# Kernel tuning notes

Measured on AMD Instinct MI355X. Metric: run time of the kernel, lower is better.

## Reference

```python
import jax, jax.numpy as jnp
import numpy as np

N_NODES = 100000
N_EDGES = 1600000
N_CLIQUES = 250000
HIDDEN = 128
HEADS = 4
D_K = 32          # attention_ratio
ATT_DIM = HEADS * D_K  # 128


def setup_inputs() -> dict:
    key = jax.random.key(0)
    ks = jax.random.split(key, 12)
    x = jax.random.normal(ks[0], (N_NODES, HIDDEN), dtype=jnp.float32)
    edge_index = jax.random.randint(ks[1], (2, N_EDGES), 0, N_NODES)
    d0_index = jax.random.randint(ks[2], (2, 2 * N_EDGES), 0, N_NODES)
    twoClique_index = jax.random.randint(ks[3], (3, N_CLIQUES), 0, N_NODES)
    d1_index = jax.random.randint(ks[4], (2, 3 * N_CLIQUES), 0, N_EDGES)
    # learned params (torch nn.Linear uses W [out,in]; we store transposed [in,out])
    scale = 0.01
    Qw = jax.random.normal(ks[5], (HIDDEN, ATT_DIM), dtype=jnp.float32) * scale
    Qb = jax.random.normal(ks[6], (ATT_DIM,), dtype=jnp.float32) * scale
    Kw = jax.random.normal(ks[7], (HIDDEN, ATT_DIM), dtype=jnp.float32) * scale
    Kb = jax.random.normal(ks[8], (ATT_DIM,), dtype=jnp.float32) * scale
    Vw = jax.random.normal(ks[9], (HIDDEN, ATT_DIM), dtype=jnp.float32) * scale
    Vb = jax.random.normal(ks[10], (ATT_DIM,), dtype=jnp.float32) * scale
    return {"x": x, "edge_index": edge_index, "d0_index": d0_index,
            "twoClique_index": twoClique_index, "d1_index": d1_index,
            "Qw": Qw, "Qb": Qb, "Kw": Kw, "Kb": Kb, "Vw": Vw, "Vb": Vb}


def reference(x, edge_index, d0_index, twoClique_index, d1_index,
              Qw, Qb, Kw, Kb, Vw, Vb):
    # projections: [N, H, d_k]
    q = (x @ Qw + Qb).reshape(-1, HEADS, D_K)
    k = (x @ Kw + Kb).reshape(-1, HEADS, D_K)
    v = (x @ Vw + Vb).reshape(-1, HEADS, D_K)

    i, j, kk = twoClique_index[0], twoClique_index[1], twoClique_index[2]
    q_i, q_j, q_k = q[i], q[j], q[kk]
    k_i, k_j, k_k = k[i], k[j], k[kk]
    v_i, v_j, v_k = v[i], v[j], v[kk]

    # symmetrized 6-term contraction, sum over d_k then mean over heads
    pre = (q_i * k_j * v_k + q_j * k_k * v_i + q_k * k_i * v_j
           + q_j * k_i * v_k + q_k * k_j * v_i + q_i * k_k * v_j).sum(-1) * (1.0 / 6.0)
    pre = pre.mean(axis=-1)            # [nCliques]
    diagA2 = jnp.exp(pre)              # use_squareplus=False

    # clique -> edge: each clique contributes its score to its 3 edges
    clique_score_per_edge = jnp.repeat(diagA2, 3)           # [3*nCliques]
    diagA1 = jax.ops.segment_sum(clique_score_per_edge, d1_index[1],
                                 num_segments=edge_index.shape[1])

    # edge -> node: each edge contributes its score to its 2 endpoints
    edge_score_per_node = jnp.repeat(diagA1, 2)             # [2*nEdges]
    diagA0 = jax.ops.segment_sum(edge_score_per_node, d0_index[1],
                                 num_segments=N_NODES)
    return (diagA0, diagA1, diagA2)
```

## Files before the change

### kernel.cpp

```cpp
#include <hip/hip_runtime.h>

#define N_NODES   100000
#define N_EDGES   1600000
#define N_CLIQUES 250000
#define FIXSCALE  8388608.0f
#define INVSCALE  1.1920928955078125e-7f

typedef unsigned short ushort8v __attribute__((ext_vector_type(8)));
typedef __bf16 bf16x8 __attribute__((ext_vector_type(8)));
typedef float f32x4 __attribute__((ext_vector_type(4)));
typedef float f32x2 __attribute__((ext_vector_type(2)));

__device__ __forceinline__ float bf2f(unsigned short u) {
    return __uint_as_float(((unsigned int)u) << 16);
}
__device__ __forceinline__ unsigned short f2bf(float f) {
    unsigned int u = __float_as_uint(f);
    u += 0x7FFFu + ((u >> 16) & 1u);
    return (unsigned short)(u >> 16);
}

__global__ __launch_bounds__(256) void prep_weights(
    const float* __restrict__ Qw, const float* __restrict__ Kw,
    const float* __restrict__ Vw, unsigned short* __restrict__ wt)
{
    int idx = blockIdx.x * 256 + threadIdx.x;
    int t = idx >> 14;
    int rem = idx & 16383;
    int col = rem >> 7;
    int k = rem & 127;
    const float* W = (t == 0) ? Qw : ((t == 1) ? Kw : Vw);
    wt[idx] = f2bf(W[k * 128 + col]);
}

__global__ __launch_bounds__(256) void proj_mfma(
    const float* __restrict__ x,
    const unsigned short* __restrict__ wt,
    const float* __restrict__ Qb, const float* __restrict__ Kb,
    const float* __restrict__ Vb,
    unsigned char* __restrict__ qkv8)
{
    __shared__ unsigned short wS[128 * 128];

    const int tid  = threadIdx.x;
    const int lane = tid & 63;
    const int w    = tid >> 6;
    const int node0 = blockIdx.x * 64;
    const int arow = lane & 15;
    const int kg   = lane >> 4;

    bf16x8 afrag[4];
    const int myNode = node0 + w * 16 + arow;
    const bool valid = myNode < N_NODES;
    const float* xrow = x + (size_t)myNode * 128;
    #pragma unroll
    for (int kt = 0; kt < 4; ++kt) {
        float4 v0, v1;
        const int kbase = kt * 32 + kg * 8;
        if (valid) {
            v0 = *(const float4*)(xrow + kbase);
            v1 = *(const float4*)(xrow + kbase + 4);
        } else {
            v0.x = v0.y = v0.z = v0.w = 0.f;
            v1.x = v1.y = v1.z = v1.w = 0.f;
        }
        ushort8v u;
        u[0] = f2bf(v0.x); u[1] = f2bf(v0.y); u[2] = f2bf(v0.z); u[3] = f2bf(v0.w);
        u[4] = f2bf(v1.x); u[5] = f2bf(v1.y); u[6] = f2bf(v1.z); u[7] = f2bf(v1.w);
        afrag[kt] = __builtin_bit_cast(bf16x8, u);
    }

    float biasr[3][8];
    #pragma unroll
    for (int t = 0; t < 3; ++t) {
        const float* Bp = (t == 0) ? Qb : ((t == 1) ? Kb : Vb);
        #pragma unroll
        for (int c = 0; c < 8; ++c) biasr[t][c] = Bp[c * 16 + arow];
    }

    for (int t = 0; t < 3; ++t) {
        __syncthreads();
        {
            const unsigned short* src = wt + t * 16384;
            #pragma unroll
            for (int it = 0; it < 8; ++it) {
                int i   = tid + it * 256;
                int col = i >> 4;
                int ko  = i & 15;
                *(ushort8v*)&wS[col * 128 + (ko ^ (col & 7)) * 8] =
                    *(const ushort8v*)(src + i * 8);
            }
        }
        __syncthreads();

        f32x4 acc[8];
        #pragma unroll
        for (int c = 0; c < 8; ++c) acc[c] = (f32x4){0.f, 0.f, 0.f, 0.f};

        #pragma unroll
        for (int kt = 0; kt < 4; ++kt) {
            const int chunk = kt * 4 + kg;
            #pragma unroll
            for (int c = 0; c < 8; ++c) {
                const int col = c * 16 + arow;
                ushort8v bu = *(const ushort8v*)&wS[col * 128 + (chunk ^ (col & 7)) * 8];
                acc[c] = __builtin_amdgcn_mfma_f32_16x16x32_bf16(
                    afrag[kt], __builtin_bit_cast(bf16x8, bu), acc[c], 0, 0, 0);
            }
        }

        #pragma unroll
        for (int r = 0; r < 4; ++r) {
            int node = node0 + w * 16 + kg * 4 + r;
            if (node < N_NODES) {
                int lo0 = __builtin_amdgcn_cvt_pk_fp8_f32(
                    acc[0][r] + biasr[t][0], acc[1][r] + biasr[t][1], 0, false);
                unsigned int w0 = (unsigned int)__builtin_amdgcn_cvt_pk_fp8_f32(
                    acc[2][r] + biasr[t][2], acc[3][r] + biasr[t][3], lo0, true);
                int lo1 = __builtin_amdgcn_cvt_pk_fp8_f32(
                    acc[4][r] + biasr[t][4], acc[5][r] + biasr[t][5], 0, false);
                unsigned int w1 = (unsigned int)__builtin_amdgcn_cvt_pk_fp8_f32(
                    acc[6][r] + biasr[t][6], acc[7][r] + biasr[t][7], lo1, true);
                uint2 o; o.x = w0; o.y = w1;
                *(uint2*)(qkv8 + (size_t)node * 384 + t * 128 + arow * 8) = o;
            }
        }
    }
}

#define DEC4(w_, a_) { f32x2 lo_ = __builtin_amdgcn_cvt_pk_f32_fp8((int)(w_), false); \
                       f32x2 hi_ = __builtin_amdgcn_cvt_pk_f32_fp8((int)(w_), true);  \
                       a_[0] = lo_[0]; a_[1] = lo_[1]; a_[2] = hi_[0]; a_[3] = hi_[1]; }

__global__ __launch_bounds__(256) void clique_kernel(
    const unsigned char* __restrict__ qkv8,
    const int* __restrict__ tci,
    const int* __restrict__ d1row1,
    const int* __restrict__ d0row1,
    float* __restrict__ outA1,
    float* __restrict__ outA2,
    unsigned int* __restrict__ a0c)
{
    const int tid = threadIdx.x;
    const int lane8 = tid & 7;
    const int cliq = (blockIdx.x * 256 + tid) >> 3;
    if (cliq >= N_CLIQUES) return;

    const int ni = tci[cliq];
    const int nj = tci[N_CLIQUES + cliq];
    const int nk = tci[2 * N_CLIQUES + cliq];
    const int d0 = lane8 * 16;

    const unsigned char* bi = qkv8 + (size_t)ni * 384 + d0;
    const unsigned char* bj = qkv8 + (size_t)nj * 384 + d0;
    const unsigned char* bk = qkv8 + (size_t)nk * 384 + d0;

    const uint4 rQi = *(const uint4*)(bi);
    const uint4 rKi = *(const uint4*)(bi + 128);
    const uint4 rVi = *(const uint4*)(bi + 256);
    const uint4 rQj = *(const uint4*)(bj);
    const uint4 rKj = *(const uint4*)(bj + 128);
    const uint4 rVj = *(const uint4*)(bj + 256);
    const uint4 rQk = *(const uint4*)(bk);
    const uint4 rKk = *(const uint4*)(bk + 128);
    const uint4 rVk = *(const uint4*)(bk + 256);

    float s = 0.f;
    #pragma unroll
    for (int c = 0; c < 4; ++c) {
        unsigned int wQi = ((const unsigned int*)&rQi)[c];
        unsigned int wKi = ((const unsigned int*)&rKi)[c];
        unsigned int wVi = ((const unsigned int*)&rVi)[c];
        unsigned int wQj = ((const unsigned int*)&rQj)[c];
        unsigned int wKj = ((const unsigned int*)&rKj)[c];
        unsigned int wVj = ((const unsigned int*)&rVj)[c];
        unsigned int wQk = ((const unsigned int*)&rQk)[c];
        unsigned int wKk = ((const unsigned int*)&rKk)[c];
        unsigned int wVk = ((const unsigned int*)&rVk)[c];
        float qi_[4], ki_[4], vi_[4], qj_[4], kj_[4], vj_[4], qk_[4], kk_[4], vk_[4];
        DEC4(wQi, qi_); DEC4(wKi, ki_); DEC4(wVi, vi_);
        DEC4(wQj, qj_); DEC4(wKj, kj_); DEC4(wVj, vj_);
        DEC4(wQk, qk_); DEC4(wKk, kk_); DEC4(wVk, vk_);
        #pragma unroll
        for (int d = 0; d < 4; ++d) {
            s = fmaf(qi_[d], fmaf(kj_[d], vk_[d], kk_[d] * vj_[d]), s);
            s = fmaf(qj_[d], fmaf(kk_[d], vi_[d], ki_[d] * vk_[d]), s);
            s = fmaf(qk_[d], fmaf(ki_[d], vj_[d], kj_[d] * vi_[d]), s);
        }
    }
    s += __shfl_xor(s, 1);
    s += __shfl_xor(s, 2);
    s += __shfl_xor(s, 4);

    float score = expf(s * (1.0f / 24.0f));
    if (lane8 == 0) outA2[cliq] = score;
    if (lane8 < 3) {
        int e = d1row1[3 * cliq + lane8];
        atomicAdd(outA1 + e, score);
        int2 tg = *(const int2*)(d0row1 + 2 * (size_t)e);
        unsigned int fx = (unsigned int)__float2uint_rn(score * FIXSCALE);
        unsigned int* base = a0c + (size_t)(cliq & 7) * N_NODES;
        atomicAdd(base + tg.x, fx);
        atomicAdd(base + tg.y, fx);
    }
}

__global__ __launch_bounds__(256) void combineA0_kernel(
    const unsigned int* __restrict__ a0c, float* __restrict__ outA0)
{
    int n = blockIdx.x * 256 + threadIdx.x;
    if (n < N_NODES) {
        unsigned int s = 0;
        #pragma unroll
        for (int c = 0; c < 8; ++c) s += a0c[(size_t)c * N_NODES + n];
        outA0[n] = (float)s * INVSCALE;
    }
}

extern "C" void kernel_launch(void* const* d_in, const int* in_sizes, int n_in,
                              void* d_out, int out_size, void* d_ws, size_t ws_size,
                              hipStream_t stream)
{
    const float* x  = (const float*)d_in[0];
    const int*   d0i = (const int*)d_in[2];
    const int*   tci = (const int*)d_in[3];
    const int*   d1i = (const int*)d_in[4];
    const float* Qw = (const float*)d_in[5];
    const float* Qb = (const float*)d_in[6];
    const float* Kw = (const float*)d_in[7];
    const float* Kb = (const float*)d_in[8];
    const float* Vw = (const float*)d_in[9];
    const float* Vb = (const float*)d_in[10];

    const int* d0row1 = d0i + 2 * (size_t)N_EDGES;
    const int* d1row1 = d1i + 3 * (size_t)N_CLIQUES;

    const size_t QKV_B = (size_t)N_NODES * 384;
    const size_t WT_B  = 3 * 128 * 128 * 2;
    unsigned char* qkv8 = (unsigned char*)d_ws;
    unsigned short* wt  = (unsigned short*)(qkv8 + QKV_B);
    unsigned int* a0c = (unsigned int*)(qkv8 + QKV_B + WT_B);

    float* outA0 = (float*)d_out;
    float* outA1 = outA0 + N_NODES;
    float* outA2 = outA0 + N_NODES + N_EDGES;

    hipMemsetAsync(outA1, 0, (size_t)N_EDGES * 4, stream);
    hipMemsetAsync(a0c, 0, (size_t)8 * N_NODES * 4, stream);
    prep_weights<<<192, 256, 0, stream>>>(Qw, Kw, Vw, wt);
    proj_mfma<<<(N_NODES + 63) / 64, 256, 0, stream>>>(x, wt, Qb, Kb, Vb, qkv8);
    clique_kernel<<<(N_CLIQUES * 8 + 255) / 256, 256, 0, stream>>>(
        qkv8, tci, d1row1, d0row1, outA1, outA2, a0c);
    combineA0_kernel<<<(N_NODES + 255) / 256, 256, 0, stream>>>(a0c, outA0);
}
```

Baseline: 147.2 us.

## Use fixed-point integer atomics for edge scores and enlarge projection blocks

Edge-score accumulation now does integer atomicAdd on a fixed-point workspace buffer instead of float atomicAdd on the output, and a new decode kernel converts that buffer back to float. The projection kernel moves to 512-thread blocks covering 128 nodes, so each block loads the shared weight tile half as often per node, and bias loads move inside the per-matrix loop. This adds one extra kernel launch and another 6.4 MB of memory traffic, and it makes edge sums deterministic but quantized.

```diff
diff --git a/kernel.cpp b/kernel.cpp
--- a/kernel.cpp
+++ b/kernel.cpp
@@ -33,7 +33,7 @@
     wt[idx] = f2bf(W[k * 128 + col]);
 }
 
-__global__ __launch_bounds__(256) void proj_mfma(
+__global__ __launch_bounds__(512, 6) void proj_mfma(
     const float* __restrict__ x,
     const unsigned short* __restrict__ wt,
     const float* __restrict__ Qb, const float* __restrict__ Kb,
@@ -45,7 +45,7 @@
     const int tid  = threadIdx.x;
     const int lane = tid & 63;
     const int w    = tid >> 6;
-    const int node0 = blockIdx.x * 64;
+    const int node0 = blockIdx.x * 128;
     const int arow = lane & 15;
     const int kg   = lane >> 4;
 
@@ -70,27 +70,23 @@
         afrag[kt] = __builtin_bit_cast(bf16x8, u);
     }
 
-    float biasr[3][8];
-    #pragma unroll
-    for (int t = 0; t < 3; ++t) {
-        const float* Bp = (t == 0) ? Qb : ((t == 1) ? Kb : Vb);
-        #pragma unroll
-        for (int c = 0; c < 8; ++c) biasr[t][c] = Bp[c * 16 + arow];
-    }
-
     for (int t = 0; t < 3; ++t) {
         __syncthreads();
         {
             const unsigned short* src = wt + t * 16384;
             #pragma unroll
-            for (int it = 0; it < 8; ++it) {
-                int i   = tid + it * 256;
+            for (int it = 0; it < 4; ++it) {
+                int i   = tid + it * 512;
                 int col = i >> 4;
                 int ko  = i & 15;
                 *(ushort8v*)&wS[col * 128 + (ko ^ (col & 7)) * 8] =
                     *(const ushort8v*)(src + i * 8);
             }
         }
+        const float* Bp = (t == 0) ? Qb : ((t == 1) ? Kb : Vb);
+        float biasr[8];
+        #pragma unroll
+        for (int c = 0; c < 8; ++c) biasr[c] = Bp[c * 16 + arow];
         __syncthreads();
 
         f32x4 acc[8];
@@ -114,13 +110,13 @@
             int node = node0 + w * 16 + kg * 4 + r;
             if (node < N_NODES) {
                 int lo0 = __builtin_amdgcn_cvt_pk_fp8_f32(
-                    acc[0][r] + biasr[t][0], acc[1][r] + biasr[t][1], 0, false);
+                    acc[0][r] + biasr[0], acc[1][r] + biasr[1], 0, false);
                 unsigned int w0 = (unsigned int)__builtin_amdgcn_cvt_pk_fp8_f32(
-                    acc[2][r] + biasr[t][2], acc[3][r] + biasr[t][3], lo0, true);
+                    acc[2][r] + biasr[2], acc[3][r] + biasr[3], lo0, true);
                 int lo1 = __builtin_amdgcn_cvt_pk_fp8_f32(
-                    acc[4][r] + biasr[t][4], acc[5][r] + biasr[t][5], 0, false);
+                    acc[4][r] + biasr[4], acc[5][r] + biasr[5], 0, false);
                 unsigned int w1 = (unsigned int)__builtin_amdgcn_cvt_pk_fp8_f32(
-                    acc[6][r] + biasr[t][6], acc[7][r] + biasr[t][7], lo1, true);
+                    acc[6][r] + biasr[6], acc[7][r] + biasr[7], lo1, true);
                 uint2 o; o.x = w0; o.y = w1;
                 *(uint2*)(qkv8 + (size_t)node * 384 + t * 128 + arow * 8) = o;
             }
@@ -137,7 +133,7 @@
     const int* __restrict__ tci,
     const int* __restrict__ d1row1,
     const int* __restrict__ d0row1,
-    float* __restrict__ outA1,
+    unsigned int* __restrict__ a1u,
     float* __restrict__ outA2,
     unsigned int* __restrict__ a0c)
 {
@@ -196,12 +192,27 @@
     if (lane8 == 0) outA2[cliq] = score;
     if (lane8 < 3) {
         int e = d1row1[3 * cliq + lane8];
-        atomicAdd(outA1 + e, score);
+        unsigned int fx = (unsigned int)__float2uint_rn(score * FIXSCALE);
+        atomicAdd(a1u + e, fx);
         int2 tg = *(const int2*)(d0row1 + 2 * (size_t)e);
-        unsigned int fx = (unsigned int)__float2uint_rn(score * FIXSCALE);
         unsigned int* base = a0c + (size_t)(cliq & 7) * N_NODES;
         atomicAdd(base + tg.x, fx);
         atomicAdd(base + tg.y, fx);
+    }
+}
+
+__global__ __launch_bounds__(256) void decodeA1_kernel(
+    const unsigned int* __restrict__ a1u, float* __restrict__ outA1)
+{
+    int e4 = blockIdx.x * 256 + threadIdx.x;
+    if (e4 * 4 < N_EDGES) {
+        uint4 v = *(const uint4*)(a1u + e4 * 4);
+        float4 o;
+        o.x = (float)v.x * INVSCALE;
+        o.y = (float)v.y * INVSCALE;
+        o.z = (float)v.z * INVSCALE;
+        o.w = (float)v.w * INVSCALE;
+        *(float4*)(outA1 + e4 * 4) = o;
     }
 }
 
@@ -237,19 +248,22 @@
 
     const size_t QKV_B = (size_t)N_NODES * 384;
     const size_t WT_B  = 3 * 128 * 128 * 2;
+    const size_t A1U_B = (size_t)N_EDGES * 4;
     unsigned char* qkv8 = (unsigned char*)d_ws;
     unsigned short* wt  = (unsigned short*)(qkv8 + QKV_B);
-    unsigned int* a0c = (unsigned int*)(qkv8 + QKV_B + WT_B);
+    unsigned int* a1u = (unsigned int*)(qkv8 + QKV_B + WT_B);
+    unsigned int* a0c = (unsigned int*)(qkv8 + QKV_B + WT_B + A1U_B);
 
     float* outA0 = (float*)d_out;
     float* outA1 = outA0 + N_NODES;
     float* outA2 = outA0 + N_NODES + N_EDGES;
 
-    hipMemsetAsync(outA1, 0, (size_t)N_EDGES * 4, stream);
+    hipMemsetAsync(a1u, 0, A1U_B, stream);
     hipMemsetAsync(a0c, 0, (size_t)8 * N_NODES * 4, stream);
     prep_weights<<<192, 256, 0, stream>>>(Qw, Kw, Vw, wt);
-    proj_mfma<<<(N_NODES + 63) / 64, 256, 0, stream>>>(x, wt, Qb, Kb, Vb, qkv8);
+    proj_mfma<<<(N_NODES + 127) / 128, 512, 0, stream>>>(x, wt, Qb, Kb, Vb, qkv8);
     clique_kernel<<<(N_CLIQUES * 8 + 255) / 256, 256, 0, stream>>>(
-        qkv8, tci, d1row1, d0row1, outA1, outA2, a0c);
+        qkv8, tci, d1row1, d0row1, a1u, outA2, a0c);
+    decodeA1_kernel<<<(N_EDGES / 4 + 255) / 256, 256, 0, stream>>>(a1u, outA1);
     combineA0_kernel<<<(N_NODES + 255) / 256, 256, 0, stream>>>(a0c, outA0);
 }
```

Measured after the change: 164.3 us. 11.6% more time.
